# Kernel optimization log

Measured on AMD Instinct MI355X. Metric: run time of the kernel, lower is better.

## Reference

```python
import jax, jax.numpy as jnp
import numpy as np

N_ROIS = 2000
FH, FW, C = 50, 50, 512
PH, PW = 7, 7
N_CLASS = 21
IMG = 800
FC_IN = PH * PW * C  # 25088
FC_OUT = 4096


def crop_and_resize(img, boxes, ph, pw):
    """Faithful jax port of tf.image.crop_and_resize (bilinear, extrapolation 0).
    img: [H, W, C]; boxes: [N, 4] normalized (y1, x1, y2, x2). Returns [N, ph, pw, C]."""
    H, W, _ = img.shape
    y1, x1, y2, x2 = boxes[:, 0], boxes[:, 1], boxes[:, 2], boxes[:, 3]
    iy = jnp.arange(ph, dtype=boxes.dtype)
    ix = jnp.arange(pw, dtype=boxes.dtype)
    # TF sampling grid: in_y = y1*(H-1) + i * (y2-y1)*(H-1)/(crop_h-1)
    in_y = y1[:, None] * (H - 1) + iy[None, :] * ((y2 - y1)[:, None] * (H - 1) / (ph - 1))  # [N, ph]
    in_x = x1[:, None] * (W - 1) + ix[None, :] * ((x2 - x1)[:, None] * (W - 1) / (pw - 1))  # [N, pw]
    y0f = jnp.floor(in_y); x0f = jnp.floor(in_x)
    ylerp = (in_y - y0f)[:, :, None, None]   # [N, ph, 1, 1]
    xlerp = (in_x - x0f)[:, None, :, None]   # [N, 1, pw, 1]
    y0 = jnp.clip(y0f, 0, H - 1).astype(jnp.int32)
    y1i = jnp.clip(y0f + 1, 0, H - 1).astype(jnp.int32)
    x0 = jnp.clip(x0f, 0, W - 1).astype(jnp.int32)
    x1i = jnp.clip(x0f + 1, 0, W - 1).astype(jnp.int32)

    def gather(yi, xi):  # [N,ph],[N,pw] -> [N,ph,pw,C]
        return img[yi[:, :, None], xi[:, None, :]]

    top = gather(y0, x0) * (1 - xlerp) + gather(y0, x1i) * xlerp
    bot = gather(y1i, x0) * (1 - xlerp) + gather(y1i, x1i) * xlerp
    out = top * (1 - ylerp) + bot * ylerp
    valid = ((in_y >= 0) & (in_y <= H - 1))[:, :, None] & ((in_x >= 0) & (in_x <= W - 1))[:, None, :]
    return jnp.where(valid[..., None], out, jnp.zeros((), out.dtype))


def setup_inputs() -> dict:
    key = jax.random.key(0)
    kf, ky, kx, k1, k2, k3, k4, k5, k6 = jax.random.split(key, 9)
    feature = jax.random.normal(kf, (1, FH, FW, C), dtype=jnp.float32)
    # valid boxes in original-image coordinates: y1<y2, x1<x2 within [0, IMG]
    ys = jnp.sort(jax.random.uniform(ky, (N_ROIS, 2), dtype=jnp.float32) * IMG, axis=1)
    xs = jnp.sort(jax.random.uniform(kx, (N_ROIS, 2), dtype=jnp.float32) * IMG, axis=1)
    rois = jnp.stack([ys[:, 0], xs[:, 0], ys[:, 1], xs[:, 1]], axis=1)
    W_fc = jax.random.normal(k1, (FC_IN, FC_OUT), dtype=jnp.float32) * 0.01
    b_fc = jnp.zeros((FC_OUT,), dtype=jnp.float32)
    W_loc = jax.random.normal(k3, (FC_OUT, N_CLASS * 4), dtype=jnp.float32) * 0.01
    b_loc = jnp.zeros((N_CLASS * 4,), dtype=jnp.float32)
    W_score = jax.random.normal(k5, (FC_OUT, N_CLASS), dtype=jnp.float32) * 0.01
    b_score = jnp.zeros((N_CLASS,), dtype=jnp.float32)
    return {"feature": feature, "rois": rois, "img_h": IMG, "img_w": IMG,
            "W_fc": W_fc, "b_fc": b_fc, "W_loc": W_loc, "b_loc": b_loc,
            "W_score": W_score, "b_score": b_score}


def reference(feature, rois, img_h, img_w, W_fc, b_fc, W_loc, b_loc, W_score, b_score):
    norm = jnp.array([img_h, img_w, img_h, img_w], dtype=jnp.float32)
    boxes = rois / norm                      # normalized [y1,x1,y2,x2]
    pool = crop_and_resize(feature[0], boxes, PH, PW)  # [N, 7, 7, 512]
    flat = pool.reshape(rois.shape[0], -1)   # [N, 25088]
    fc = flat @ W_fc + b_fc                  # [N, 4096]
    roi_cls_locs = fc @ W_loc + b_loc        # [N, 84]
    roi_scores = fc @ W_score + b_score      # [N, 21]
    return roi_cls_locs, roi_scores
```

## Files before the change

kernel.cpp:

```cpp
#include <hip/hip_runtime.h>
#include <stdint.h>


typedef float          f32x4 __attribute__((ext_vector_type(4)));
typedef __bf16         bfx8  __attribute__((ext_vector_type(8)));
typedef unsigned short u16x8 __attribute__((ext_vector_type(8)));
typedef unsigned short u16x4 __attribute__((ext_vector_type(4)));

#define KBIG 25088
#define NMID 4096
#define NROIS 2000
#define G1BLOCKS 784
#define SPLITS 28

__device__ __forceinline__ unsigned short f2bf(float f) {
  unsigned int u = __float_as_uint(f);
  return (unsigned short)((u + 0x7fffu + ((u >> 16) & 1u)) >> 16);
}

__device__ __forceinline__ void gll16(const void* g, void* l) {
  __builtin_amdgcn_global_load_lds(
      (const __attribute__((address_space(1))) void*)(uintptr_t)(g),
      (__attribute__((address_space(3))) void*)(uintptr_t)(l), 16, 0, 0);
}

__global__ __launch_bounds__(256) void k_prep(const float* __restrict__ Wl,
                                              const float* __restrict__ Ws,
                                              const float* __restrict__ bfc,
                                              const float* __restrict__ bl,
                                              const float* __restrict__ bs,
                                              unsigned short* __restrict__ WcatT,
                                              float* __restrict__ bc) {
  if (blockIdx.x < 2048) {
    int idx = blockIdx.x * 256 + threadIdx.x;
    int c = idx >> 12, k = idx & 4095;
    float v = 0.0f;
    if (c < 84)       v = Wl[k * 84 + c];
    else if (c < 105) v = Ws[k * 21 + (c - 84)];
    WcatT[idx] = f2bf(v);
  } else {
    int c = blockIdx.x - 2048;
    int t = threadIdx.x;
    __shared__ float red[256];
    float p = 0.0f;
    if (c < 105) {
      for (int k = t; k < 4096; k += 256) {
        float w = (c < 84) ? Wl[k * 84 + c] : Ws[k * 21 + (c - 84)];
        p += bfc[k] * w;
      }
    }
    red[t] = p;
    __syncthreads();
    for (int s = 128; s > 0; s >>= 1) {
      if (t < s) red[t] += red[t + s];
      __syncthreads();
    }
    if (t == 0) {
      float bias = (c < 84) ? bl[c] : (c < 105 ? bs[c - 84] : 0.0f);
      bc[c] = (c < 105) ? (red[0] + bias) : 0.0f;
    }
  }
}

__global__ __launch_bounds__(256) void k_pool_gemm1(
    const float* __restrict__ F, const float* __restrict__ rois,
    const int* __restrict__ ihp, const int* __restrict__ iwp,
    unsigned short* __restrict__ A,
    const float* __restrict__ Wfc, const unsigned short* __restrict__ WcatT,
    unsigned short* __restrict__ WcT) {
  const int t = threadIdx.x;
  if (blockIdx.x < G1BLOCKS) {
    __shared__ __align__(16) char sA[4096];
    __shared__ __align__(16) char sB[16384];
    const int lane = t & 63, wid = t >> 6;
    const int l15 = lane & 15, l4 = lane >> 4;
    const int mtile = blockIdx.x * 32;
    const int jlog = (t & 7) ^ ((t >> 3) & 7);
    f32x4 acc[2][2] = {};

    const int arow = t >> 3;
    const int aj = t & 7;
    const float* aptr = Wfc + (size_t)(mtile + arow) * NMID + aj * 8;
    char* awr = sA + arow * 128 + ((aj ^ (arow & 7)) << 4);

    f32x4 v0 = *(const f32x4*)(aptr);
    f32x4 v1 = *(const f32x4*)(aptr + 4);
    for (int ks = 0; ks < 64; ++ks) {
      u16x8 p;
#pragma unroll
      for (int i = 0; i < 4; ++i) { p[i] = f2bf(v0[i]); p[i + 4] = f2bf(v1[i]); }
      *(u16x8*)awr = p;
#pragma unroll
      for (int c = 0; c < 4; ++c)
        gll16(WcatT + (size_t)(c * 32 + (t >> 3)) * NMID + ks * 64 + jlog * 8,
              sB + c * 4096 + wid * 1024);
      __syncthreads();
      if (ks < 63) {
        v0 = *(const f32x4*)(aptr + (ks + 1) * 64);
        v1 = *(const f32x4*)(aptr + (ks + 1) * 64 + 4);
      }
#pragma unroll
      for (int kh = 0; kh < 2; ++kh) {
        bfx8 af[2], bfr[2];
#pragma unroll
        for (int mi = 0; mi < 2; ++mi) {
          const int row = mi * 16 + l15;
          af[mi] = *(const bfx8*)(sA + row * 128 + ((((kh << 2) + l4) ^ (row & 7)) << 4));
        }
#pragma unroll
        for (int ni = 0; ni < 2; ++ni) {
          const int row = wid * 32 + ni * 16 + l15;
          bfr[ni] = *(const bfx8*)(sB + row * 128 + ((((kh << 2) + l4) ^ (row & 7)) << 4));
        }
#pragma unroll
        for (int mi = 0; mi < 2; ++mi)
#pragma unroll
          for (int ni = 0; ni < 2; ++ni)
            acc[mi][ni] = __builtin_amdgcn_mfma_f32_16x16x32_bf16(af[mi], bfr[ni], acc[mi][ni], 0, 0, 0);
      }
      __syncthreads();
    }
#pragma unroll
    for (int mi = 0; mi < 2; ++mi)
#pragma unroll
      for (int ni = 0; ni < 2; ++ni) {
        const int gm0 = mtile + mi * 16 + l4 * 4;
        const int gn = wid * 32 + ni * 16 + l15;
        u16x4 pk;
#pragma unroll
        for (int i = 0; i < 4; ++i) pk[i] = f2bf(acc[mi][ni][i]);
        *(u16x4*)(WcT + (size_t)gn * KBIG + gm0) = pk;
      }
  } else {
    const int r = blockIdx.x - G1BLOCKS;
    const float ih = (float)ihp[0], iw = (float)iwp[0];
    const float y1 = rois[r * 4 + 0] / ih;
    const float x1 = rois[r * 4 + 1] / iw;
    const float y2 = rois[r * 4 + 2] / ih;
    const float x2 = rois[r * 4 + 3] / iw;
    const float sy = (y2 - y1) * 49.0f / 6.0f;
    const float sx = (x2 - x1) * 49.0f / 6.0f;
    const int ch = t * 2;
    unsigned int* __restrict__ Arow = (unsigned int*)(A + (size_t)r * KBIG);
    for (int cell = 0; cell < 49; ++cell) {
      const int iy = cell / 7, ix = cell - iy * 7;
      const float in_y = y1 * 49.0f + (float)iy * sy;
      const float in_x = x1 * 49.0f + (float)ix * sx;
      const float y0f = floorf(in_y), x0f = floorf(in_x);
      const float yl = in_y - y0f, xl = in_x - x0f;
      const int y0  = (int)fminf(fmaxf(y0f, 0.0f), 49.0f);
      const int y1i = (int)fminf(fmaxf(y0f + 1.0f, 0.0f), 49.0f);
      const int x0  = (int)fminf(fmaxf(x0f, 0.0f), 49.0f);
      const int x1i = (int)fminf(fmaxf(x0f + 1.0f, 0.0f), 49.0f);
      const bool valid = (in_y >= 0.0f) && (in_y <= 49.0f) &&
                         (in_x >= 0.0f) && (in_x <= 49.0f);
      float2 f00 = *(const float2*)&F[(y0 * 50 + x0) * 512 + ch];
      float2 f01 = *(const float2*)&F[(y0 * 50 + x1i) * 512 + ch];
      float2 f10 = *(const float2*)&F[(y1i * 50 + x0) * 512 + ch];
      float2 f11 = *(const float2*)&F[(y1i * 50 + x1i) * 512 + ch];
      float o0 = 0.0f, o1 = 0.0f;
      if (valid) {
        float t0 = f00.x * (1.0f - xl) + f01.x * xl;
        float t1 = f00.y * (1.0f - xl) + f01.y * xl;
        float b0 = f10.x * (1.0f - xl) + f11.x * xl;
        float b1 = f10.y * (1.0f - xl) + f11.y * xl;
        o0 = t0 * (1.0f - yl) + b0 * yl;
        o1 = t1 * (1.0f - yl) + b1 * yl;
      }
      Arow[(cell * 512 + ch) >> 1] =
          (unsigned int)f2bf(o0) | ((unsigned int)f2bf(o1) << 16);
    }
  }
}

__global__ __launch_bounds__(256) void k_gemm2(const unsigned short* __restrict__ Ap,
                                               const unsigned short* __restrict__ WcT,
                                               float* __restrict__ P) {
  __shared__ __align__(16) char sA[8192];
  __shared__ __align__(16) char sB[16384];
  const int t = threadIdx.x;
  const int lane = t & 63, wid = t >> 6;
  const int wm = wid >> 1, wn = wid & 1;
  const int l15 = lane & 15, l4 = lane >> 4;
  const int mt = blockIdx.x, sp = blockIdx.y;
  const int kbase = sp * 896;
  const int jlog = (t & 7) ^ ((t >> 3) & 7);
  f32x4 acc[2][4] = {};

  int ar0 = mt * 64 + (t >> 3);
  int ar1 = ar0 + 32;
  if (ar0 > NROIS - 1) ar0 = NROIS - 1;
  if (ar1 > NROIS - 1) ar1 = NROIS - 1;
  const unsigned short* asrc0 = Ap + (size_t)ar0 * KBIG + jlog * 8;
  const unsigned short* asrc1 = Ap + (size_t)ar1 * KBIG + jlog * 8;

  for (int ks = 0; ks < 14; ++ks) {
    const int k0 = kbase + ks * 64;
    gll16(asrc0 + k0, sA + wid * 1024);
    gll16(asrc1 + k0, sA + 4096 + wid * 1024);
#pragma unroll
    for (int c = 0; c < 4; ++c)
      gll16(WcT + (size_t)(c * 32 + (t >> 3)) * KBIG + k0 + jlog * 8,
            sB + c * 4096 + wid * 1024);
    __syncthreads();
#pragma unroll
    for (int kh = 0; kh < 2; ++kh) {
      bfx8 af[2], bfr[4];
#pragma unroll
      for (int mi = 0; mi < 2; ++mi) {
        const int row = wm * 32 + mi * 16 + l15;
        af[mi] = *(const bfx8*)(sA + row * 128 + ((((kh << 2) + l4) ^ (row & 7)) << 4));
      }
#pragma unroll
      for (int ni = 0; ni < 4; ++ni) {
        const int row = wn * 64 + ni * 16 + l15;
        bfr[ni] = *(const bfx8*)(sB + row * 128 + ((((kh << 2) + l4) ^ (row & 7)) << 4));
      }
#pragma unroll
      for (int mi = 0; mi < 2; ++mi)
#pragma unroll
        for (int ni = 0; ni < 4; ++ni)
          acc[mi][ni] = __builtin_amdgcn_mfma_f32_16x16x32_bf16(af[mi], bfr[ni], acc[mi][ni], 0, 0, 0);
    }
    __syncthreads();
  }
  float* out = P + (size_t)(mt * SPLITS + sp) * 8192;
#pragma unroll
  for (int mi = 0; mi < 2; ++mi)
#pragma unroll
    for (int ni = 0; ni < 4; ++ni)
#pragma unroll
      for (int i = 0; i < 4; ++i)
        out[(wm * 32 + mi * 16 + l4 * 4 + i) * 128 + wn * 64 + ni * 16 + l15] = acc[mi][ni][i];
}

__global__ __launch_bounds__(128) void k_reduce(const float* __restrict__ P,
                                                const float* __restrict__ bc,
                                                float* __restrict__ out) {
  const int m = blockIdx.x;
  const int c = threadIdx.x;
  if (c >= 105) return;
  const int mt = m >> 6, r = m & 63;
  float sum = 0.0f;
#pragma unroll
  for (int s = 0; s < SPLITS; ++s)
    sum += P[(size_t)(mt * SPLITS + s) * 8192 + r * 128 + c];
  sum += bc[c];
  if (c < 84) out[m * 84 + c] = sum;
  else        out[168000 + m * 21 + (c - 84)] = sum;
}

extern "C" void kernel_launch(void* const* d_in, const int* in_sizes, int n_in,
                              void* d_out, int out_size, void* d_ws, size_t ws_size,
                              hipStream_t stream) {
  const float* F    = (const float*)d_in[0];
  const float* rois = (const float*)d_in[1];
  const int*   ih   = (const int*)d_in[2];
  const int*   iw   = (const int*)d_in[3];
  const float* Wfc  = (const float*)d_in[4];
  const float* bfc  = (const float*)d_in[5];
  const float* Wl   = (const float*)d_in[6];
  const float* bl   = (const float*)d_in[7];
  const float* Ws   = (const float*)d_in[8];
  const float* bs   = (const float*)d_in[9];
  (void)in_sizes; (void)n_in; (void)out_size; (void)ws_size;

  char* ws = (char*)d_ws;
  unsigned short* Apool = (unsigned short*)(ws);
  unsigned short* WcatT = (unsigned short*)(ws + 100352000);
  unsigned short* WcT   = (unsigned short*)(ws + 101400576);
  float*          bc    = (float*)(ws + 107823104);
  float*          P     = (float*)(ws + 107823616);
  float*          out   = (float*)d_out;

  k_prep      <<<2176, 256, 0, stream>>>(Wl, Ws, bfc, bl, bs, WcatT, bc);
  k_pool_gemm1<<<G1BLOCKS + NROIS, 256, 0, stream>>>(F, rois, ih, iw, Apool,
                                                     Wfc, WcatT, WcT);
  k_gemm2     <<<dim3(32, SPLITS), 256, 0, stream>>>(Apool, WcT, P);
  k_reduce    <<<NROIS, 128, 0, stream>>>(P, bc, out);
}
```

Baseline: 235.7 us.

## Double-buffer LDS in both GEMMs and split-K the weight-fold GEMM

The first GEMM (folding W_fc with the concatenated head weights) now uses 64-row tiles with split-K of two. Its global loads are software-pipelined through register prefetch and double-buffered LDS, using explicit vmcnt waits and raw barriers. The fp32 partials go to a new workspace and a new add-and-convert kernel sums them into bf16. The second GEMM gets the same double-buffered LDS pipeline with partial vmcnt waits so loads overlap MFMA work. This costs an extra kernel launch, extra fp32 partial traffic and larger LDS use that may lower occupancy.

```diff
diff --git a/kernel.cpp b/kernel.cpp
--- a/kernel.cpp
+++ b/kernel.cpp
@@ -5,7 +5,6 @@
 typedef float          f32x4 __attribute__((ext_vector_type(4)));
 typedef __bf16         bfx8  __attribute__((ext_vector_type(8)));
 typedef unsigned short u16x8 __attribute__((ext_vector_type(8)));
-typedef unsigned short u16x4 __attribute__((ext_vector_type(4)));
 
 #define KBIG 25088
 #define NMID 4096
@@ -62,75 +61,96 @@
   }
 }
 
-__global__ __launch_bounds__(256) void k_pool_gemm1(
+__global__ __launch_bounds__(256, 3) void k_pool_gemm1(
     const float* __restrict__ F, const float* __restrict__ rois,
     const int* __restrict__ ihp, const int* __restrict__ iwp,
     unsigned short* __restrict__ A,
     const float* __restrict__ Wfc, const unsigned short* __restrict__ WcatT,
-    unsigned short* __restrict__ WcT) {
+    float* __restrict__ Pg1) {
   const int t = threadIdx.x;
+  __shared__ __align__(16) char sB[32768];
   if (blockIdx.x < G1BLOCKS) {
-    __shared__ __align__(16) char sA[4096];
-    __shared__ __align__(16) char sB[16384];
     const int lane = t & 63, wid = t >> 6;
     const int l15 = lane & 15, l4 = lane >> 4;
-    const int mtile = blockIdx.x * 32;
+    const int mt = blockIdx.x >> 1, sp = blockIdx.x & 1;
+    const int m0 = mt * 64;
+    const int kbase = sp * 2048;
     const int jlog = (t & 7) ^ ((t >> 3) & 7);
-    f32x4 acc[2][2] = {};
-
-    const int arow = t >> 3;
-    const int aj = t & 7;
-    const float* aptr = Wfc + (size_t)(mtile + arow) * NMID + aj * 8;
-    char* awr = sA + arow * 128 + ((aj ^ (arow & 7)) << 4);
-
-    f32x4 v0 = *(const f32x4*)(aptr);
-    f32x4 v1 = *(const f32x4*)(aptr + 4);
-    for (int ks = 0; ks < 64; ++ks) {
-      u16x8 p;
-#pragma unroll
-      for (int i = 0; i < 4; ++i) { p[i] = f2bf(v0[i]); p[i + 4] = f2bf(v1[i]); }
-      *(u16x8*)awr = p;
-#pragma unroll
-      for (int c = 0; c < 4; ++c)
-        gll16(WcatT + (size_t)(c * 32 + (t >> 3)) * NMID + ks * 64 + jlog * 8,
-              sB + c * 4096 + wid * 1024);
-      __syncthreads();
-      if (ks < 63) {
-        v0 = *(const f32x4*)(aptr + (ks + 1) * 64);
-        v1 = *(const f32x4*)(aptr + (ks + 1) * 64 + 4);
-      }
-#pragma unroll
-      for (int kh = 0; kh < 2; ++kh) {
-        bfx8 af[2], bfr[2];
-#pragma unroll
-        for (int mi = 0; mi < 2; ++mi) {
-          const int row = mi * 16 + l15;
-          af[mi] = *(const bfx8*)(sA + row * 128 + ((((kh << 2) + l4) ^ (row & 7)) << 4));
+    f32x4 acc[8] = {};
+    f32x4 rA[4], rB[4];
+
+    const float* aptr = Wfc + (size_t)(m0 + wid * 16 + l15) * NMID + kbase + l4 * 8;
+
+    auto stageB = [&](int c, int off) {
+#pragma unroll
+      for (int q = 0; q < 4; ++q)
+        gll16(WcatT + (size_t)(q * 32 + (t >> 3)) * NMID + kbase + c * 64 + jlog * 8,
+              sB + off + q * 4096 + wid * 1024);
+    };
+    auto loadA = [&](f32x4* dst, int c) {
+      dst[0] = *(const f32x4*)(aptr + c * 64);
+      dst[1] = *(const f32x4*)(aptr + c * 64 + 4);
+      dst[2] = *(const f32x4*)(aptr + c * 64 + 32);
+      dst[3] = *(const f32x4*)(aptr + c * 64 + 36);
+    };
+    auto cvtA = [&](bfx8& af0, bfx8& af1, const f32x4* r) {
+      u16x8 p0, p1;
+#pragma unroll
+      for (int i = 0; i < 4; ++i) {
+        p0[i] = f2bf(r[0][i]); p0[i + 4] = f2bf(r[1][i]);
+        p1[i] = f2bf(r[2][i]); p1[i + 4] = f2bf(r[3][i]);
+      }
+      af0 = *(bfx8*)&p0; af1 = *(bfx8*)&p1;
+    };
+    auto compute = [&](int off, bfx8 af0, bfx8 af1) {
+#pragma unroll
+      for (int kk = 0; kk < 2; ++kk) {
+        bfx8 bfr[8];
+#pragma unroll
+        for (int nt = 0; nt < 8; ++nt) {
+          const int row = nt * 16 + l15;
+          bfr[nt] = *(const bfx8*)(sB + off + row * 128 + ((((kk << 2) + l4) ^ (row & 7)) << 4));
         }
-#pragma unroll
-        for (int ni = 0; ni < 2; ++ni) {
-          const int row = wid * 32 + ni * 16 + l15;
-          bfr[ni] = *(const bfx8*)(sB + row * 128 + ((((kh << 2) + l4) ^ (row & 7)) << 4));
-        }
-#pragma unroll
-        for (int mi = 0; mi < 2; ++mi)
-#pragma unroll
-          for (int ni = 0; ni < 2; ++ni)
-            acc[mi][ni] = __builtin_amdgcn_mfma_f32_16x16x32_bf16(af[mi], bfr[ni], acc[mi][ni], 0, 0, 0);
-      }
-      __syncthreads();
-    }
-#pragma unroll
-    for (int mi = 0; mi < 2; ++mi)
-#pragma unroll
-      for (int ni = 0; ni < 2; ++ni) {
-        const int gm0 = mtile + mi * 16 + l4 * 4;
-        const int gn = wid * 32 + ni * 16 + l15;
-        u16x4 pk;
-#pragma unroll
-        for (int i = 0; i < 4; ++i) pk[i] = f2bf(acc[mi][ni][i]);
-        *(u16x4*)(WcT + (size_t)gn * KBIG + gm0) = pk;
-      }
+        const bfx8 af = kk ? af1 : af0;
+#pragma unroll
+        for (int nt = 0; nt < 8; ++nt)
+          acc[nt] = __builtin_amdgcn_mfma_f32_16x16x32_bf16(af, bfr[nt], acc[nt], 0, 0, 0);
+      }
+    };
+
+    stageB(0, 0);
+    __builtin_amdgcn_sched_barrier(0);
+    loadA(rA, 0);
+    loadA(rB, 1);
+    for (int cc = 0; cc < 16; ++cc) {
+      const int c0 = cc * 2;
+      bfx8 af0, af1;
+      cvtA(af0, af1, rA);
+      stageB(c0 + 1, 16384);
+      __builtin_amdgcn_sched_barrier(0);
+      loadA(rA, (c0 + 2 < 32) ? c0 + 2 : 31);
+      asm volatile("s_waitcnt vmcnt(12)" ::: "memory");
+      __builtin_amdgcn_s_barrier();
+      __builtin_amdgcn_sched_barrier(0);
+      compute(0, af0, af1);
+      __builtin_amdgcn_s_barrier();
+      cvtA(af0, af1, rB);
+      stageB((c0 + 2 < 32) ? c0 + 2 : 31, 0);
+      __builtin_amdgcn_sched_barrier(0);
+      loadA(rB, (c0 + 3 < 32) ? c0 + 3 : 31);
+      asm volatile("s_waitcnt vmcnt(12)" ::: "memory");
+      __builtin_amdgcn_s_barrier();
+      __builtin_amdgcn_sched_barrier(0);
+      compute(16384, af0, af1);
+      __builtin_amdgcn_s_barrier();
+    }
+    asm volatile("s_waitcnt vmcnt(0)" ::: "memory");
+#pragma unroll
+    for (int nt = 0; nt < 8; ++nt) {
+      const int n = nt * 16 + l15;
+      float* dst = Pg1 + ((size_t)sp * 128 + n) * KBIG + m0 + wid * 16 + l4 * 4;
+      *(f32x4*)dst = acc[nt];
+    }
   } else {
     const int r = blockIdx.x - G1BLOCKS;
     const float ih = (float)ihp[0], iw = (float)iwp[0];
@@ -173,11 +193,26 @@
   }
 }
 
+__global__ __launch_bounds__(256) void k_addcvt(const float* __restrict__ Pg1,
+                                                unsigned short* __restrict__ WcT) {
+  const size_t i = ((size_t)blockIdx.x * 256 + threadIdx.x) * 8;
+  f32x4 a0 = *(const f32x4*)(Pg1 + i);
+  f32x4 a1 = *(const f32x4*)(Pg1 + i + 4);
+  f32x4 b0 = *(const f32x4*)(Pg1 + 3211264 + i);
+  f32x4 b1 = *(const f32x4*)(Pg1 + 3211264 + i + 4);
+  u16x8 o;
+#pragma unroll
+  for (int j = 0; j < 4; ++j) {
+    o[j]     = f2bf(a0[j] + b0[j]);
+    o[j + 4] = f2bf(a1[j] + b1[j]);
+  }
+  *(u16x8*)(WcT + i) = o;
+}
+
 __global__ __launch_bounds__(256) void k_gemm2(const unsigned short* __restrict__ Ap,
                                                const unsigned short* __restrict__ WcT,
                                                float* __restrict__ P) {
-  __shared__ __align__(16) char sA[8192];
-  __shared__ __align__(16) char sB[16384];
+  __shared__ __align__(16) char S[49152];
   const int t = threadIdx.x;
   const int lane = t & 63, wid = t >> 6;
   const int wm = wid >> 1, wn = wid & 1;
@@ -194,27 +229,28 @@
   const unsigned short* asrc0 = Ap + (size_t)ar0 * KBIG + jlog * 8;
   const unsigned short* asrc1 = Ap + (size_t)ar1 * KBIG + jlog * 8;
 
-  for (int ks = 0; ks < 14; ++ks) {
-    const int k0 = kbase + ks * 64;
-    gll16(asrc0 + k0, sA + wid * 1024);
-    gll16(asrc1 + k0, sA + 4096 + wid * 1024);
-#pragma unroll
-    for (int c = 0; c < 4; ++c)
-      gll16(WcT + (size_t)(c * 32 + (t >> 3)) * KBIG + k0 + jlog * 8,
-            sB + c * 4096 + wid * 1024);
-    __syncthreads();
+  auto stage2 = [&](int c, int off) {
+    const int k0 = kbase + c * 64;
+    gll16(asrc0 + k0, S + off + wid * 1024);
+    gll16(asrc1 + k0, S + off + 4096 + wid * 1024);
+#pragma unroll
+    for (int q = 0; q < 4; ++q)
+      gll16(WcT + (size_t)(q * 32 + (t >> 3)) * KBIG + k0 + jlog * 8,
+            S + off + 8192 + q * 4096 + wid * 1024);
+  };
+  auto compute2 = [&](int off) {
 #pragma unroll
     for (int kh = 0; kh < 2; ++kh) {
       bfx8 af[2], bfr[4];
 #pragma unroll
       for (int mi = 0; mi < 2; ++mi) {
         const int row = wm * 32 + mi * 16 + l15;
-        af[mi] = *(const bfx8*)(sA + row * 128 + ((((kh << 2) + l4) ^ (row & 7)) << 4));
+        af[mi] = *(const bfx8*)(S + off + row * 128 + ((((kh << 2) + l4) ^ (row & 7)) << 4));
       }
 #pragma unroll
       for (int ni = 0; ni < 4; ++ni) {
         const int row = wn * 64 + ni * 16 + l15;
-        bfr[ni] = *(const bfx8*)(sB + row * 128 + ((((kh << 2) + l4) ^ (row & 7)) << 4));
+        bfr[ni] = *(const bfx8*)(S + off + 8192 + row * 128 + ((((kh << 2) + l4) ^ (row & 7)) << 4));
       }
 #pragma unroll
       for (int mi = 0; mi < 2; ++mi)
@@ -222,8 +258,25 @@
         for (int ni = 0; ni < 4; ++ni)
           acc[mi][ni] = __builtin_amdgcn_mfma_f32_16x16x32_bf16(af[mi], bfr[ni], acc[mi][ni], 0, 0, 0);
     }
-    __syncthreads();
+  };
+
+  stage2(0, 0);
+  for (int cc = 0; cc < 7; ++cc) {
+    const int c0 = cc * 2;
+    stage2(c0 + 1, 24576);
+    asm volatile("s_waitcnt vmcnt(6)" ::: "memory");
+    __builtin_amdgcn_s_barrier();
+    __builtin_amdgcn_sched_barrier(0);
+    compute2(0);
+    __builtin_amdgcn_s_barrier();
+    stage2((c0 + 2 < 14) ? c0 + 2 : 13, 0);
+    asm volatile("s_waitcnt vmcnt(6)" ::: "memory");
+    __builtin_amdgcn_s_barrier();
+    __builtin_amdgcn_sched_barrier(0);
+    compute2(24576);
+    __builtin_amdgcn_s_barrier();
   }
+  asm volatile("s_waitcnt vmcnt(0)" ::: "memory");
   float* out = P + (size_t)(mt * SPLITS + sp) * 8192;
 #pragma unroll
   for (int mi = 0; mi < 2; ++mi)
@@ -271,11 +324,13 @@
   unsigned short* WcT   = (unsigned short*)(ws + 101400576);
   float*          bc    = (float*)(ws + 107823104);
   float*          P     = (float*)(ws + 107823616);
+  float*          Pg1   = (float*)(ws + 137183744);
   float*          out   = (float*)d_out;
 
   k_prep      <<<2176, 256, 0, stream>>>(Wl, Ws, bfc, bl, bs, WcatT, bc);
   k_pool_gemm1<<<G1BLOCKS + NROIS, 256, 0, stream>>>(F, rois, ih, iw, Apool,
-                                                     Wfc, WcatT, WcT);
+                                                     Wfc, WcatT, Pg1);
+  k_addcvt    <<<1568, 256, 0, stream>>>(Pg1, WcT);
   k_gemm2     <<<dim3(32, SPLITS), 256, 0, stream>>>(Apool, WcT, P);
   k_reduce    <<<NROIS, 128, 0, stream>>>(P, bc, out);
 }
```

After: 232.9 us. No clear change (-1.2%).
